# Performance work log

Hardware: AMD Instinct MI355X
Metric: run time of the kernel (lower is better)

Reference implementation:

```python
import jax, jax.numpy as jnp
import numpy as np

NEG = -1e30  # finite stand-in for -inf to keep logsumexp NaN-free


def setup_inputs() -> dict:
    key = jax.random.key(0)
    k1, k2 = jax.random.split(key)
    B, T, C, L = 1024, 256, 128, 48
    # ctc_batch_cost expects softmax probabilities over C classes (blank = C-1)
    y_pred = jax.nn.softmax(jax.random.normal(k1, (B, T, C), dtype=jnp.float32), axis=-1)
    labels = jax.random.randint(k2, (B, L), 0, C - 1, dtype=jnp.int32)  # values in [0, C-2]
    return {"y_pred": y_pred, "labels": labels}


def _lse3(a, b, c):
    m = jnp.maximum(jnp.maximum(a, b), c)
    return m + jnp.log(jnp.exp(a - m) + jnp.exp(b - m) + jnp.exp(c - m))


def reference(y_pred, labels):
    """CTC loss matching keras.backend.ctc_batch_cost (blank = num_classes-1),
    with full input_length=T and label_length=L as in CTCLayer.call.
    Returns per-example loss of shape [B, 1]."""
    eps = 1e-7  # keras.backend.epsilon()
    logp = jnp.log(y_pred + eps)              # [B, T, C]
    B, T, C = y_pred.shape
    L = labels.shape[1]
    S = 2 * L + 1                             # extended label length (blanks interleaved)
    blank = C - 1

    # extended label: blank, l1, blank, l2, ..., lL, blank  -> [B, S]
    ext = jnp.full((B, S), blank, dtype=labels.dtype).at[:, 1::2].set(labels)
    # transition s-2 -> s allowed iff ext[s] != blank and ext[s] != ext[s-2]
    can_skip = jnp.concatenate(
        [jnp.zeros((B, 2), dtype=bool), (ext[:, 2:] != blank) & (ext[:, 2:] != ext[:, :-2])],
        axis=1)                               # [B, S]

    # log-probs gathered at extended-label symbols: [T, B, S]
    lpe = jnp.take_along_axis(jnp.transpose(logp, (1, 0, 2)),
                              jnp.broadcast_to(ext[None], (T, B, S)), axis=2)

    alpha0 = (jnp.full((B, S), NEG, dtype=logp.dtype)
              .at[:, 0].set(lpe[0, :, 0])
              .at[:, 1].set(lpe[0, :, 1]))

    pad1 = jnp.full((B, 1), NEG, dtype=logp.dtype)
    pad2 = jnp.full((B, 2), NEG, dtype=logp.dtype)

    def step(alpha, lp_t):
        a2 = jnp.concatenate([pad1, alpha[:, :-1]], axis=1)
        a3 = jnp.where(can_skip, jnp.concatenate([pad2, alpha[:, :-2]], axis=1), NEG)
        alpha = _lse3(alpha, a2, a3) + lp_t
        return alpha, None

    alphaT, _ = jax.lax.scan(step, alpha0, lpe[1:])
    loss = -jnp.logaddexp(alphaT[:, S - 1], alphaT[:, S - 2])  # end at last blank or last label
    return loss[:, None]                       # [B, 1], matching ctc_batch_cost
```

## Files before the change

kernel.cpp:

```cpp
#include <hip/hip_runtime.h>


#define TT 256
#define CC 128
#define LL 48
#define CH 16
#define NC (TT / CH)

typedef float f32x4 __attribute__((ext_vector_type(4)));

template<int CTRL>
__device__ __forceinline__ float dpp_mv(float x) {
    union { float f; int i; } u, r;
    u.f = x;
    r.i = __builtin_amdgcn_update_dpp(0, u.i, CTRL, 0xF, 0xF, false);
    return r.f;
}
__device__ __forceinline__ float rdlane(float x, int l) {
    union { float f; int i; } u, r;
    u.f = x;
    r.i = __builtin_amdgcn_readlane(u.i, l);
    return r.f;
}

__global__ __launch_bounds__(192) void ctc_fwd_v11(
    const float* __restrict__ y,
    const int* __restrict__ labels,
    float* __restrict__ out)
{
    __shared__ float ring[4][CH * CC];
    const int lane = threadIdx.x & 63;
    const int w = threadIdx.x >> 6;
    const int b = blockIdx.x;
    const float EPS = 1e-7f;

    if (w != 0) {
        const f32x4* p4 = (const f32x4*)(y + (size_t)b * TT * CC);
        const int jb = (w - 1) * 4;
        f32x4 RA[4], RB[4], RC[4];

#define LOADP(set, c_) do {                                               \
    _Pragma("unroll")                                                     \
    for (int _jj = 0; _jj < 4; ++_jj)                                     \
        (set)[_jj] = p4[(size_t)(c_) * (CH * CC / 4) + (jb + _jj) * 64 + lane]; \
    } while (0)

#define PITER(set, c_) do {                                               \
    float* _s = ring[(c_) & 3];                                           \
    _Pragma("unroll")                                                     \
    for (int _jj = 0; _jj < 4; ++_jj)                                     \
        *(f32x4*)&_s[((jb + _jj) * 64 + lane) * 4] = (set)[_jj];          \
    asm volatile("s_waitcnt lgkmcnt(0)" ::: "memory");                    \
    __builtin_amdgcn_sched_barrier(0);                                    \
    __builtin_amdgcn_s_barrier();                     \
    __builtin_amdgcn_sched_barrier(0);                                    \
    if ((c_) + 3 < NC) LOADP(set, (c_) + 3);                              \
    } while (0)

        LOADP(RA, 0); LOADP(RB, 1); LOADP(RC, 2);
        PITER(RA, 0);  PITER(RB, 1);  PITER(RC, 2);
        PITER(RA, 3);  PITER(RB, 4);  PITER(RC, 5);
        PITER(RA, 6);  PITER(RB, 7);  PITER(RC, 8);
        PITER(RA, 9);  PITER(RB, 10); PITER(RC, 11);
        PITER(RA, 12); PITER(RB, 13); PITER(RC, 14);
        PITER(RA, 15);
#undef LOADP
#undef PITER
    } else {
        int lab = CC - 1;
        if (lane < LL) lab = labels[b * LL + lane];
        const int labprev = __shfl_up(lab, 1);
        const float csf = ((lane > 0) && (lane < LL) && (lab != labprev)) ? 1.0f : 0.0f;

        float a0 = (lane == 0) ? 1.0f : 0.0f;
        float a1 = 0.0f;
        int lg = 0;

#define STEP(plv, pbv) do {                                               \
    const float _pp = dpp_mv<0x138>(a1);       \
    const float _a0o = a0;                                                \
    a0 = (_a0o + _pp) * (pbv);                                            \
    a1 = (a1 + _a0o + csf * _pp) * (plv);                                 \
    } while (0)

#define RESCALE do {                                                      \
    float _m = fmaxf(a0, a1);                                             \
    _m = fmaxf(_m, dpp_mv<0x111>(_m));                     \
    _m = fmaxf(_m, dpp_mv<0x112>(_m));                     \
    _m = fmaxf(_m, dpp_mv<0x114>(_m));                     \
    _m = fmaxf(_m, dpp_mv<0x118>(_m));                     \
    _m = fmaxf(_m, dpp_mv<0x142>(_m));                  \
    _m = fmaxf(_m, dpp_mv<0x143>(_m));        \
    const float _mm = rdlane(_m, 63);                                     \
    int _e; (void)frexpf(_mm, &_e);                                       \
    a0 = ldexpf(a0, -_e);                                                 \
    a1 = ldexpf(a1, -_e);                                                 \
    lg += _e;                                                             \
    } while (0)

#define CITER(c_) do {                                                    \
    __builtin_amdgcn_s_barrier();                 \
    __builtin_amdgcn_sched_barrier(0);                                    \
    const float* _s = ring[(c_) & 3];                                     \
    float _pl[CH], _pb[CH];                                               \
    _Pragma("unroll")                                                     \
    for (int _r = 0; _r < CH; ++_r) {                                     \
        _pl[_r] = _s[_r * CC + lab] + EPS;           \
        _pb[_r] = _s[_r * CC + (CC - 1)] + EPS;       \
    }                                                                     \
    _Pragma("unroll")                                                     \
    for (int _r = 0; _r < CH; ++_r) {                                     \
        STEP(_pl[_r], _pb[_r]);                                           \
        if ((_r & 7) == 7) RESCALE;                                       \
    } } while (0)

        CITER(0);  CITER(1);  CITER(2);  CITER(3);
        CITER(4);  CITER(5);  CITER(6);  CITER(7);
        CITER(8);  CITER(9);  CITER(10); CITER(11);
        CITER(12); CITER(13); CITER(14); CITER(15);

        const float v95 = rdlane(a1, 47);
        const float v96 = rdlane(a0, 48);
        if (lane == 0) {
            const float s = fmaxf(v95 + v96, 1e-37f);
            out[b] = -(__logf(s) + (float)lg * 0.69314718056f);
        }
#undef STEP
#undef RESCALE
#undef CITER
    }
}

extern "C" void kernel_launch(void* const* d_in, const int* in_sizes, int n_in,
                              void* d_out, int out_size, void* d_ws, size_t ws_size,
                              hipStream_t stream) {
    const float* y = (const float*)d_in[0];
    const int* labels = (const int*)d_in[1];
    float* out = (float*)d_out;
    const int B = in_sizes[0] / (TT * CC);
    ctc_fwd_v11<<<B, 192, 0, stream>>>(y, labels, out);
}
```

Baseline: 26.99 us.

## Stream chunks with direct global-to-LDS loads from a single producer wave

The two producer waves that loaded chunks into registers and then stored them to shared memory are replaced by one wave. That wave issues 16-byte global_load_lds transfers straight into the four-slot ring. Synchronisation now waits on vmcnt with three chunks in flight, and the block shrinks from 192 to 128 threads. The aim is to cut the register round trip and LDS store instructions and to free resources for higher occupancy. The cost is that a single wave must issue all the memory traffic, and correctness relies on vmcnt ordering covering the direct-to-LDS writes.

```diff
diff --git a/kernel.cpp b/kernel.cpp
--- a/kernel.cpp
+++ b/kernel.cpp
@@ -6,8 +6,6 @@
 #define LL 48
 #define CH 16
 #define NC (TT / CH)
-
-typedef float f32x4 __attribute__((ext_vector_type(4)));
 
 template<int CTRL>
 __device__ __forceinline__ float dpp_mv(float x) {
@@ -23,7 +21,14 @@
     return r.f;
 }
 
-__global__ __launch_bounds__(192) void ctc_fwd_v11(
+__device__ __forceinline__ void gload_lds16(const float* g, float* l) {
+    __builtin_amdgcn_global_load_lds(
+        (const __attribute__((address_space(1))) unsigned int*)(const void*)g,
+        (__attribute__((address_space(3))) unsigned int*)(void*)l,
+        16, 0, 0);
+}
+
+__global__ __launch_bounds__(128) void ctc_fwd_v14(
     const float* __restrict__ y,
     const int* __restrict__ labels,
     float* __restrict__ out)
@@ -34,38 +39,44 @@
     const int b = blockIdx.x;
     const float EPS = 1e-7f;
 
-    if (w != 0) {
-        const f32x4* p4 = (const f32x4*)(y + (size_t)b * TT * CC);
-        const int jb = (w - 1) * 4;
-        f32x4 RA[4], RB[4], RC[4];
+    if (w == 1) {
+        const float* yb = y + (size_t)b * TT * CC + lane * 4;
 
-#define LOADP(set, c_) do {                                               \
+#define GISSUE(c_) do {                                                   \
+    const float* _g = yb + (size_t)(c_) * (CH * CC);                      \
+    float* _l = ring[(c_) & 3];                                           \
     _Pragma("unroll")                                                     \
-    for (int _jj = 0; _jj < 4; ++_jj)                                     \
-        (set)[_jj] = p4[(size_t)(c_) * (CH * CC / 4) + (jb + _jj) * 64 + lane]; \
+    for (int _k = 0; _k < 8; ++_k)                                        \
+        gload_lds16(_g + _k * 256, _l + _k * 256);         \
     } while (0)
 
-#define PITER(set, c_) do {                                               \
-    float* _s = ring[(c_) & 3];                                           \
-    _Pragma("unroll")                                                     \
-    for (int _jj = 0; _jj < 4; ++_jj)                                     \
-        *(f32x4*)&_s[((jb + _jj) * 64 + lane) * 4] = (set)[_jj];          \
-    asm volatile("s_waitcnt lgkmcnt(0)" ::: "memory");                    \
-    __builtin_amdgcn_sched_barrier(0);                                    \
-    __builtin_amdgcn_s_barrier();                     \
-    __builtin_amdgcn_sched_barrier(0);                                    \
-    if ((c_) + 3 < NC) LOADP(set, (c_) + 3);                              \
+#define SB __builtin_amdgcn_sched_barrier(0)
+#define HANDSHAKE(wstr) do {                                              \
+    asm volatile("s_waitcnt " wstr ::: "memory");                         \
+    SB;                                                                   \
+    __builtin_amdgcn_s_barrier();                                         \
+    SB;                                                                   \
     } while (0)
 
-        LOADP(RA, 0); LOADP(RB, 1); LOADP(RC, 2);
-        PITER(RA, 0);  PITER(RB, 1);  PITER(RC, 2);
-        PITER(RA, 3);  PITER(RB, 4);  PITER(RC, 5);
-        PITER(RA, 6);  PITER(RB, 7);  PITER(RC, 8);
-        PITER(RA, 9);  PITER(RB, 10); PITER(RC, 11);
-        PITER(RA, 12); PITER(RB, 13); PITER(RC, 14);
-        PITER(RA, 15);
-#undef LOADP
-#undef PITER
+        GISSUE(0); GISSUE(1); GISSUE(2);
+        HANDSHAKE("vmcnt(16)"); GISSUE(3);
+        HANDSHAKE("vmcnt(16)"); GISSUE(4);
+        HANDSHAKE("vmcnt(16)"); GISSUE(5);
+        HANDSHAKE("vmcnt(16)"); GISSUE(6);
+        HANDSHAKE("vmcnt(16)"); GISSUE(7);
+        HANDSHAKE("vmcnt(16)"); GISSUE(8);
+        HANDSHAKE("vmcnt(16)"); GISSUE(9);
+        HANDSHAKE("vmcnt(16)"); GISSUE(10);
+        HANDSHAKE("vmcnt(16)"); GISSUE(11);
+        HANDSHAKE("vmcnt(16)"); GISSUE(12);
+        HANDSHAKE("vmcnt(16)"); GISSUE(13);
+        HANDSHAKE("vmcnt(16)"); GISSUE(14);
+        HANDSHAKE("vmcnt(16)"); GISSUE(15);
+        HANDSHAKE("vmcnt(16)");
+        HANDSHAKE("vmcnt(8)");
+        HANDSHAKE("vmcnt(0)");
+#undef GISSUE
+#undef HANDSHAKE
     } else {
         int lab = CC - 1;
         if (lane < LL) lab = labels[b * LL + lane];
@@ -99,14 +110,14 @@
     } while (0)
 
 #define CITER(c_) do {                                                    \
-    __builtin_amdgcn_s_barrier();                 \
+    __builtin_amdgcn_s_barrier();             \
     __builtin_amdgcn_sched_barrier(0);                                    \
     const float* _s = ring[(c_) & 3];                                     \
     float _pl[CH], _pb[CH];                                               \
     _Pragma("unroll")                                                     \
     for (int _r = 0; _r < CH; ++_r) {                                     \
         _pl[_r] = _s[_r * CC + lab] + EPS;           \
-        _pb[_r] = _s[_r * CC + (CC - 1)] + EPS;       \
+        _pb[_r] = _s[_r * CC + (CC - 1)] + EPS;    \
     }                                                                     \
     _Pragma("unroll")                                                     \
     for (int _r = 0; _r < CH; ++_r) {                                     \
@@ -138,5 +149,5 @@
     const int* labels = (const int*)d_in[1];
     float* out = (float*)d_out;
     const int B = in_sizes[0] / (TT * CC);
-    ctc_fwd_v11<<<B, 192, 0, stream>>>(y, labels, out);
+    ctc_fwd_v14<<<B, 128, 0, stream>>>(y, labels, out);
 }
```

Result: no change. 26.93 us (-0.2%).
